# Optimization experiments

Hardware: AMD Instinct MI355X
Metric: run time of the kernel (lower is better)

Reference implementation:

```python
import jax, jax.numpy as jnp
import numpy as np

N = 50000      # nodes
E = 800000     # directed edges (avg degree 16)
IN, HID, OUT = 256, 128, 16


def setup_inputs() -> dict:
    key = jax.random.key(0)
    ks = jax.random.split(key, 8)
    x = jax.random.normal(ks[0], (N, IN), dtype=jnp.float32)
    edge_index = jax.random.randint(ks[1], (2, E), 0, N)
    W1 = jax.random.normal(ks[2], (IN, HID), dtype=jnp.float32) * (1.0 / np.sqrt(IN))
    b1 = jnp.zeros((HID,), jnp.float32)
    W2 = jax.random.normal(ks[3], (HID, HID), dtype=jnp.float32) * (1.0 / np.sqrt(HID))
    b2 = jnp.zeros((HID,), jnp.float32)
    Wc = jax.random.normal(ks[4], (HID, OUT), dtype=jnp.float32) * (1.0 / np.sqrt(HID))
    bc = jnp.zeros((OUT,), jnp.float32)
    return {"x": x, "W1": W1, "b1": b1, "W2": W2, "b2": b2,
            "Wc": Wc, "bc": bc, "edge_index": edge_index, "conv_time": 30}


def _gcn_norm(edge_index, n, dtype):
    # add self-loops, compute symmetric GCN normalization D^{-1/2}(A+I)D^{-1/2}
    loops = jnp.arange(n)
    src = jnp.concatenate([edge_index[0], loops])
    dst = jnp.concatenate([edge_index[1], loops])
    deg = jax.ops.segment_sum(jnp.ones_like(dst, dtype=dtype), dst, num_segments=n)
    dinv = jnp.where(deg > 0, jax.lax.rsqrt(deg), jnp.zeros_like(deg))
    norm = dinv[src] * dinv[dst]          # [E+N] edge weights
    return src, dst, norm


def _propagate(h, src, dst, norm, n, hops):
    # hops is a static Python int (conv_time)
    for _ in range(hops):
        h = jax.ops.segment_sum(h[src] * norm[:, None], dst, num_segments=n)
    return h


def reference(x, W1, b1, W2, b2, Wc, bc, edge_index, conv_time):
    n = x.shape[0]
    src, dst, norm = _gcn_norm(edge_index, n, x.dtype)
    # conv1: linear only (conv_time = 0)
    h = jax.nn.relu(x @ W1 + b1)
    # dropout is identity in eval mode
    # conv2: linear + conv_time hops of normalized propagation
    h = _propagate(h @ W2 + b2, src, dst, norm, n, int(conv_time))
    h = jax.nn.relu(h)
    # cls: linear + 1 hop
    h = _propagate(h @ Wc + bc, src, dst, norm, n, 1)
    return h
```

## Files before the change

kernel.cpp:

```cpp
#include <hip/hip_runtime.h>
#include <hip/hip_fp16.h>

#define NNODES 50000
#define NEDGES 800000
#define IN_F   256
#define HID_F  128
#define OUT_F  16
#define HOPS   30
#define MPAD   50048

typedef unsigned int u32;
typedef _Float16 f16;
typedef f16 f16x8 __attribute__((ext_vector_type(8)));
typedef float f32x4 __attribute__((ext_vector_type(4)));

union U32H2 { u32 u; __half2 h; };

__device__ inline float2 upk(u32 v) {
    U32H2 t; t.u = v;
    return __half22float2(t.h);
}
__device__ inline u32 pk2(float a, float b) {
    U32H2 t; t.h = __floats2half2_rn(a, b);
    return t.u;
}


__global__ void k_init_deg(int* __restrict__ deg, int n) {
    int i = blockIdx.x * blockDim.x + threadIdx.x;
    if (i < n) deg[i] = 1;
}

__global__ void k_count(const int* __restrict__ dst, int* __restrict__ deg, int e) {
    int i = blockIdx.x * blockDim.x + threadIdx.x;
    if (i < e) atomicAdd(&deg[dst[i]], 1);
}

__global__ void k_dinv(const int* __restrict__ deg, float* __restrict__ dinv, int n) {
    int i = blockIdx.x * blockDim.x + threadIdx.x;
    if (i < n) dinv[i] = rsqrtf((float)deg[i]);
}

__global__ void k_scan1(const int* __restrict__ deg, int* __restrict__ bsums, int n) {
    __shared__ int sh[256];
    int tid = threadIdx.x;
    int i = blockIdx.x * 256 + tid;
    sh[tid] = (i < n) ? deg[i] : 0;
    __syncthreads();
    for (int ofs = 128; ofs > 0; ofs >>= 1) {
        if (tid < ofs) sh[tid] += sh[tid + ofs];
        __syncthreads();
    }
    if (tid == 0) bsums[blockIdx.x] = sh[0];
}

__global__ void k_scan2(int* __restrict__ bsums, int nb, int* __restrict__ rp, int n) {
    if (threadIdx.x == 0 && blockIdx.x == 0) {
        int run = 0;
        for (int b = 0; b < nb; ++b) { int t = bsums[b]; bsums[b] = run; run += t; }
        rp[n] = run;
    }
}

__global__ void k_scan3(const int* __restrict__ deg, const int* __restrict__ bsums,
                        int* __restrict__ rp, int* __restrict__ cursor, int n) {
    __shared__ int sh[256];
    int tid = threadIdx.x;
    int i = blockIdx.x * 256 + tid;
    int v = (i < n) ? deg[i] : 0;
    sh[tid] = v;
    __syncthreads();
    for (int ofs = 1; ofs < 256; ofs <<= 1) {
        int t = 0;
        if (tid >= ofs) t = sh[tid - ofs];
        __syncthreads();
        sh[tid] += t;
        __syncthreads();
    }
    if (i < n) {
        int excl = sh[tid] - v + bsums[blockIdx.x];
        rp[i] = excl;
        cursor[i] = excl;
    }
}

__global__ void k_scatter(const int* __restrict__ src, const int* __restrict__ dst,
                          const float* __restrict__ dinv, int* __restrict__ cursor,
                          int2* __restrict__ ew, int e, int n) {
    int t = blockIdx.x * blockDim.x + threadIdx.x;
    if (t < e) {
        int s = src[t], d = dst[t];
        int pos = atomicAdd(&cursor[d], 1);
        ew[pos] = make_int2(s, __float_as_int(dinv[s] * dinv[d]));
    } else if (t < e + n) {
        int i = t - e;
        int pos = atomicAdd(&cursor[i], 1);
        float di = dinv[i];
        ew[pos] = make_int2(i, __float_as_int(di * di));
    }
}

__global__ void k_sortwave(const int* __restrict__ rp, int2* __restrict__ ew, int n) {
    int node = blockIdx.x * 4 + (threadIdx.x >> 6);
    int lane = threadIdx.x & 63;
    if (node >= n) return;
    int beg = rp[node], end = rp[node + 1];
    int deg = end - beg;
    if (deg > 64) return;
    int2 my = make_int2(0x7fffffff, 0);
    if (lane < deg) my = ew[beg + lane];
    int rank = 0;
#pragma unroll 8
    for (int k = 0; k < 64; ++k) {
        int sk = __shfl(my.x, k);
        rank += (sk < my.x) || (sk == my.x && k < lane);
    }
    if (lane < deg) ew[beg + rank] = my;
}


__global__ void k_cast_x(const float* __restrict__ in, f16* __restrict__ out, int n) {
    int i = blockIdx.x * blockDim.x + threadIdx.x;
    int stride = gridDim.x * blockDim.x;
    for (; i < n / 4; i += stride) {
        float4 v = reinterpret_cast<const float4*>(in)[i];
        f16 o[4] = {(f16)v.x, (f16)v.y, (f16)v.z, (f16)v.w};
        *reinterpret_cast<uint2*>(&reinterpret_cast<f16*>(out)[i * 4]) =
            *reinterpret_cast<uint2*>(o);
    }
}

template<int K, int NC>
__global__ void k_cast_wt(const float* __restrict__ W, f16* __restrict__ Wt) {
    int i = blockIdx.x * blockDim.x + threadIdx.x;
    if (i < K * NC) {
        int k = i / NC, c = i % NC;
        Wt[(size_t)c * K + k] = (f16)W[i];
    }
}


template<int K, bool RELU>
__global__ __launch_bounds__(256)
void k_gemm_mfma(const f16* __restrict__ A, const f16* __restrict__ Wt,
                 const float* __restrict__ b, f16* __restrict__ C, int M) {
    int wid  = threadIdx.x >> 6;
    int lane = threadIdx.x & 63;
    int rowW = blockIdx.x * 64 + wid * 16;
    int rl   = lane & 15;
    int kc   = (lane >> 4) * 8;

    f32x4 acc[8];
#pragma unroll
    for (int n = 0; n < 8; ++n) acc[n] = (f32x4)0.f;

    const f16* Arow = A + (size_t)(rowW + rl) * K;
#pragma unroll
    for (int k0 = 0; k0 < K; k0 += 32) {
        f16x8 aF = *reinterpret_cast<const f16x8*>(Arow + k0 + kc);
#pragma unroll
        for (int n = 0; n < 8; ++n) {
            f16x8 bF = *reinterpret_cast<const f16x8*>(
                Wt + (size_t)(n * 16 + rl) * K + k0 + kc);
            acc[n] = __builtin_amdgcn_mfma_f32_16x16x32_f16(aF, bF, acc[n], 0, 0, 0);
        }
    }

#pragma unroll
    for (int n = 0; n < 8; ++n) {
        int col = n * 16 + rl;
        float bias = b[col];
#pragma unroll
        for (int j = 0; j < 4; ++j) {
            int row = rowW + 4 * (lane >> 4) + j;
            if (row < M) {
                float s = acc[n][j] + bias;
                if (RELU) s = fmaxf(s, 0.f);
                C[(size_t)row * 128 + col] = (f16)s;
            }
        }
    }
}


template<bool RELU>
__global__ void k_proph(const u32* __restrict__ Hin, u32* __restrict__ Hout,
                        const int* __restrict__ rp, const int2* __restrict__ ew,
                        int n) {
    int grp  = threadIdx.x >> 4;
    int lane = threadIdx.x & 15;
    int node = blockIdx.x * 16 + grp;
    if (node >= n) return;
    int beg = rp[node], end = rp[node + 1];
    const uint4* H4 = reinterpret_cast<const uint4*>(Hin);

    float acc[8];
#pragma unroll
    for (int i = 0; i < 8; ++i) acc[i] = 0.f;

    auto body = [&](int e) {
        int2 p   = ew[e];
        float ww = __int_as_float(p.y);
        uint4 v  = H4[(size_t)p.x * 16 + lane];
        const u32* vv = reinterpret_cast<const u32*>(&v);
#pragma unroll
        for (int q = 0; q < 4; ++q) {
            float2 f = upk(vv[q]);
            acc[q * 2 + 0] += ww * f.x;
            acc[q * 2 + 1] += ww * f.y;
        }
    };

    int e = beg;
    for (; e + 1 < end; e += 2) { body(e); body(e + 1); }
    if (e < end) body(e);

    if (RELU) {
#pragma unroll
        for (int i = 0; i < 8; ++i) acc[i] = fmaxf(acc[i], 0.f);
    }
    uint4 o;
    u32* ov = reinterpret_cast<u32*>(&o);
#pragma unroll
    for (int q = 0; q < 4; ++q) ov[q] = pk2(acc[q * 2], acc[q * 2 + 1]);
    reinterpret_cast<uint4*>(Hout)[(size_t)node * 16 + lane] = o;
}


__global__ void k_cls_h(const u32* __restrict__ Ah, const float* __restrict__ Wc,
                        const float* __restrict__ bc, float* __restrict__ G, int M) {
    __shared__ float sa[64][132];
    __shared__ float4 sw4[512];
    int tid  = threadIdx.x;
    int row0 = blockIdx.x * 64;

    for (int idx = tid; idx < 512; idx += 256)
        sw4[idx] = reinterpret_cast<const float4*>(Wc)[idx];

    const uint4* A4 = reinterpret_cast<const uint4*>(Ah);
    for (int idx = tid; idx < 64 * 16; idx += 256) {
        int r = idx >> 4, c = idx & 15;
        int gr = row0 + r;
        uint4 v = (gr < M) ? A4[(size_t)gr * 16 + c]
                           : make_uint4(0u, 0u, 0u, 0u);
        float* dst = &sa[r][c * 8];
        const u32* vv = reinterpret_cast<const u32*>(&v);
#pragma unroll
        for (int q = 0; q < 4; ++q) {
            float2 f = upk(vv[q]);
            dst[q * 2 + 0] = f.x;
            dst[q * 2 + 1] = f.y;
        }
    }
    __syncthreads();

    int tc = tid & 3;
    int tr = tid >> 2;
    float4 acc = make_float4(0.f, 0.f, 0.f, 0.f);
    for (int k4 = 0; k4 < 32; ++k4) {
        float4 a = *reinterpret_cast<const float4*>(&sa[tr][k4 * 4]);
        const float* af = reinterpret_cast<const float*>(&a);
#pragma unroll
        for (int kk = 0; kk < 4; ++kk) {
            float4 wv = sw4[(k4 * 4 + kk) * 4 + tc];
            float av = af[kk];
            acc.x += av * wv.x; acc.y += av * wv.y;
            acc.z += av * wv.z; acc.w += av * wv.w;
        }
    }
    int r = row0 + tr;
    if (r < M) {
        float4 bb = reinterpret_cast<const float4*>(bc)[tc];
        acc.x += bb.x; acc.y += bb.y; acc.z += bb.z; acc.w += bb.w;
        reinterpret_cast<float4*>(G)[(size_t)r * 4 + tc] = acc;
    }
}


__global__ void k_prop16(const float* __restrict__ Gin, float* __restrict__ Out,
                         const int* __restrict__ rp, const int2* __restrict__ ew,
                         int n) {
    int g    = blockIdx.x * 64 + (threadIdx.x >> 2);
    int lane = threadIdx.x & 3;
    if (g >= n) return;
    int beg = rp[g], end = rp[g + 1];
    const float4* G4 = reinterpret_cast<const float4*>(Gin);
    float ax = 0.f, ay = 0.f, az = 0.f, aw = 0.f;
    for (int e = beg; e < end; ++e) {
        int2 p   = ew[e];
        float ww = __int_as_float(p.y);
        float4 hv = G4[(size_t)p.x * 4 + lane];
        ax += ww * hv.x; ay += ww * hv.y; az += ww * hv.z; aw += ww * hv.w;
    }
    reinterpret_cast<float4*>(Out)[(size_t)g * 4 + lane] = make_float4(ax, ay, az, aw);
}


extern "C" void kernel_launch(void* const* d_in, const int* in_sizes, int n_in,
                              void* d_out, int out_size, void* d_ws, size_t ws_size,
                              hipStream_t stream) {
    const float* x  = (const float*)d_in[0];
    const float* W1 = (const float*)d_in[1];
    const float* b1 = (const float*)d_in[2];
    const float* W2 = (const float*)d_in[3];
    const float* b2 = (const float*)d_in[4];
    const float* Wc = (const float*)d_in[5];
    const float* bc = (const float*)d_in[6];
    const int*   ei = (const int*)d_in[7];
    const int* srcp = ei;
    const int* dstp = ei + NEDGES;
    float* out = (float*)d_out;

    char* p = (char*)d_ws;
    auto alloc = [&](size_t bytes) -> char* {
        char* r = p;
        p += (bytes + 255) & ~(size_t)255;
        return r;
    };
    int*   deg    = (int*)  alloc(NNODES * 4);
    float* dinv   = (float*)alloc(NNODES * 4);
    int*   rp     = (int*)  alloc((NNODES + 1) * 4);
    int*   cursor = (int*)  alloc(NNODES * 4);
    int*   bsums  = (int*)  alloc(256 * 4);
    int2*  ew     = (int2*) alloc((size_t)(NEDGES + NNODES) * 8);
    f16*   xh     = (f16*)  alloc((size_t)MPAD * IN_F * 2);
    f16*   W1t    = (f16*)  alloc((size_t)HID_F * IN_F * 2);
    f16*   W2t    = (f16*)  alloc((size_t)HID_F * HID_F * 2);
    f16*   H0h    = (f16*)  alloc((size_t)MPAD * HID_F * 2);
    u32*   Hh0    = (u32*)  alloc((size_t)NNODES * HID_F * 2);
    u32*   Hh1    = (u32*)  alloc((size_t)NNODES * HID_F * 2);
    float* G      = (float*)alloc((size_t)NNODES * OUT_F * 4);

    const int T = 256;
    auto nb = [](int n, int t) { return (n + t - 1) / t; };

    k_init_deg<<<nb(NNODES, T), T, 0, stream>>>(deg, NNODES);
    k_count<<<nb(NEDGES, T), T, 0, stream>>>(dstp, deg, NEDGES);
    k_dinv<<<nb(NNODES, T), T, 0, stream>>>(deg, dinv, NNODES);
    int NB = nb(NNODES, 256);
    k_scan1<<<NB, 256, 0, stream>>>(deg, bsums, NNODES);
    k_scan2<<<1, 1, 0, stream>>>(bsums, NB, rp, NNODES);
    k_scan3<<<NB, 256, 0, stream>>>(deg, bsums, rp, cursor, NNODES);
    k_scatter<<<nb(NEDGES + NNODES, T), T, 0, stream>>>(srcp, dstp, dinv, cursor,
                                                        ew, NEDGES, NNODES);
    k_sortwave<<<nb(NNODES, 4), 256, 0, stream>>>(rp, ew, NNODES);

    k_cast_x<<<1024, 256, 0, stream>>>(x, xh, NNODES * IN_F);
    k_cast_wt<IN_F,  HID_F><<<nb(IN_F * HID_F, T), T, 0, stream>>>(W1, W1t);
    k_cast_wt<HID_F, HID_F><<<nb(HID_F * HID_F, T), T, 0, stream>>>(W2, W2t);

    int GB = MPAD / 64;
    k_gemm_mfma<IN_F,  true ><<<GB, 256, 0, stream>>>(xh,  W1t, b1, H0h, NNODES);
    k_gemm_mfma<HID_F, false><<<GB, 256, 0, stream>>>(H0h, W2t, b2, (f16*)Hh0, NNODES);

    u32* cur = Hh0;
    u32* nxt = Hh1;
    int PB = nb(NNODES, 16);
    for (int i = 0; i < HOPS; ++i) {
        if (i == HOPS - 1)
            k_proph<true ><<<PB, 256, 0, stream>>>(cur, nxt, rp, ew, NNODES);
        else
            k_proph<false><<<PB, 256, 0, stream>>>(cur, nxt, rp, ew, NNODES);
        u32* t = cur; cur = nxt; nxt = t;
    }

    k_cls_h<<<nb(NNODES, 64), 256, 0, stream>>>(cur, Wc, bc, G, NNODES);
    k_prop16<<<nb(NNODES, 64), 256, 0, stream>>>(G, out, rp, ew, NNODES);
}
```

Baseline: 1.122 ms.

## Fuse x cast into GEMM, defer edge weights to sort, nontemporal hop loads

```diff
diff --git a/kernel.cpp b/kernel.cpp
--- a/kernel.cpp
+++ b/kernel.cpp
@@ -10,9 +10,11 @@
 #define MPAD   50048
 
 typedef unsigned int u32;
+typedef unsigned long long u64;
 typedef _Float16 f16;
 typedef f16 f16x8 __attribute__((ext_vector_type(8)));
 typedef float f32x4 __attribute__((ext_vector_type(4)));
+typedef u32 u32x4 __attribute__((ext_vector_type(4)));
 
 union U32H2 { u32 u; __half2 h; };
 
@@ -85,48 +87,43 @@
 }
 
 __global__ void k_scatter(const int* __restrict__ src, const int* __restrict__ dst,
-                          const float* __restrict__ dinv, int* __restrict__ cursor,
-                          int2* __restrict__ ew, int e, int n) {
+                          int* __restrict__ cursor, int* __restrict__ es,
+                          int e, int n) {
     int t = blockIdx.x * blockDim.x + threadIdx.x;
     if (t < e) {
-        int s = src[t], d = dst[t];
-        int pos = atomicAdd(&cursor[d], 1);
-        ew[pos] = make_int2(s, __float_as_int(dinv[s] * dinv[d]));
+        int pos = atomicAdd(&cursor[dst[t]], 1);
+        es[pos] = src[t];
     } else if (t < e + n) {
         int i = t - e;
         int pos = atomicAdd(&cursor[i], 1);
-        float di = dinv[i];
-        ew[pos] = make_int2(i, __float_as_int(di * di));
-    }
-}
-
-__global__ void k_sortwave(const int* __restrict__ rp, int2* __restrict__ ew, int n) {
+        es[pos] = i;
+    }
+}
+
+__global__ void k_sortwave(const int* __restrict__ rp, const int* __restrict__ es,
+                           const float* __restrict__ dinv, int2* __restrict__ ew,
+                           int n) {
     int node = blockIdx.x * 4 + (threadIdx.x >> 6);
     int lane = threadIdx.x & 63;
     if (node >= n) return;
     int beg = rp[node], end = rp[node + 1];
     int deg = end - beg;
-    if (deg > 64) return;
-    int2 my = make_int2(0x7fffffff, 0);
-    if (lane < deg) my = ew[beg + lane];
-    int rank = 0;
-#pragma unroll 8
-    for (int k = 0; k < 64; ++k) {
-        int sk = __shfl(my.x, k);
-        rank += (sk < my.x) || (sk == my.x && k < lane);
-    }
-    if (lane < deg) ew[beg + rank] = my;
-}
-
-
-__global__ void k_cast_x(const float* __restrict__ in, f16* __restrict__ out, int n) {
-    int i = blockIdx.x * blockDim.x + threadIdx.x;
-    int stride = gridDim.x * blockDim.x;
-    for (; i < n / 4; i += stride) {
-        float4 v = reinterpret_cast<const float4*>(in)[i];
-        f16 o[4] = {(f16)v.x, (f16)v.y, (f16)v.z, (f16)v.w};
-        *reinterpret_cast<uint2*>(&reinterpret_cast<f16*>(out)[i * 4]) =
-            *reinterpret_cast<uint2*>(o);
+    float dd = dinv[node];
+    if (deg <= 64) {
+        int s = 0x7fffffff;
+        if (lane < deg) s = es[beg + lane];
+        int rank = 0;
+        for (int k = 0; k < deg; ++k) {
+            int sk = __shfl(s, k);
+            rank += (sk < s) || (sk == s && k < lane);
+        }
+        if (lane < deg)
+            ew[beg + rank] = make_int2(s, __float_as_int(dinv[s] * dd));
+    } else {
+        for (int t = beg + lane; t < end; t += 64) {
+            int s = es[t];
+            ew[t] = make_int2(s, __float_as_int(dinv[s] * dd));
+        }
     }
 }
 
@@ -140,9 +137,9 @@
 }
 
 
-template<int K, bool RELU>
+template<int K, bool RELU, typename TA>
 __global__ __launch_bounds__(256)
-void k_gemm_mfma(const f16* __restrict__ A, const f16* __restrict__ Wt,
+void k_gemm_mfma(const TA* __restrict__ A, const f16* __restrict__ Wt,
                  const float* __restrict__ b, f16* __restrict__ C, int M) {
     int wid  = threadIdx.x >> 6;
     int lane = threadIdx.x & 63;
@@ -154,10 +151,20 @@
 #pragma unroll
     for (int n = 0; n < 8; ++n) acc[n] = (f32x4)0.f;
 
-    const f16* Arow = A + (size_t)(rowW + rl) * K;
+    int ar = rowW + rl;
+    if (ar >= M) ar = M - 1;
+    const TA* Arow = A + (size_t)ar * K;
 #pragma unroll
     for (int k0 = 0; k0 < K; k0 += 32) {
-        f16x8 aF = *reinterpret_cast<const f16x8*>(Arow + k0 + kc);
+        f16x8 aF;
+        if constexpr (sizeof(TA) == 4) {
+            float4 v0 = *reinterpret_cast<const float4*>(Arow + k0 + kc);
+            float4 v1 = *reinterpret_cast<const float4*>(Arow + k0 + kc + 4);
+            aF[0] = (f16)v0.x; aF[1] = (f16)v0.y; aF[2] = (f16)v0.z; aF[3] = (f16)v0.w;
+            aF[4] = (f16)v1.x; aF[5] = (f16)v1.y; aF[6] = (f16)v1.z; aF[7] = (f16)v1.w;
+        } else {
+            aF = *reinterpret_cast<const f16x8*>(Arow + k0 + kc);
+        }
 #pragma unroll
         for (int n = 0; n < 8; ++n) {
             f16x8 bF = *reinterpret_cast<const f16x8*>(
@@ -192,20 +199,21 @@
     int node = blockIdx.x * 16 + grp;
     if (node >= n) return;
     int beg = rp[node], end = rp[node + 1];
-    const uint4* H4 = reinterpret_cast<const uint4*>(Hin);
+    const u32x4* H4 = reinterpret_cast<const u32x4*>(Hin);
+    const u64* ew8  = reinterpret_cast<const u64*>(ew);
 
     float acc[8];
 #pragma unroll
     for (int i = 0; i < 8; ++i) acc[i] = 0.f;
 
     auto body = [&](int e) {
-        int2 p   = ew[e];
-        float ww = __int_as_float(p.y);
-        uint4 v  = H4[(size_t)p.x * 16 + lane];
-        const u32* vv = reinterpret_cast<const u32*>(&v);
+        u64 pw   = __builtin_nontemporal_load(ew8 + e);
+        int s    = (int)(u32)pw;
+        float ww = __int_as_float((u32)(pw >> 32));
+        u32x4 v  = H4[(size_t)s * 16 + lane];
 #pragma unroll
         for (int q = 0; q < 4; ++q) {
-            float2 f = upk(vv[q]);
+            float2 f = upk(v[q]);
             acc[q * 2 + 0] += ww * f.x;
             acc[q * 2 + 1] += ww * f.y;
         }
@@ -219,11 +227,11 @@
 #pragma unroll
         for (int i = 0; i < 8; ++i) acc[i] = fmaxf(acc[i], 0.f);
     }
-    uint4 o;
-    u32* ov = reinterpret_cast<u32*>(&o);
-#pragma unroll
-    for (int q = 0; q < 4; ++q) ov[q] = pk2(acc[q * 2], acc[q * 2 + 1]);
-    reinterpret_cast<uint4*>(Hout)[(size_t)node * 16 + lane] = o;
+    u32x4 o;
+#pragma unroll
+    for (int q = 0; q < 4; ++q) o[q] = pk2(acc[q * 2], acc[q * 2 + 1]);
+    __builtin_nontemporal_store(o, reinterpret_cast<u32x4*>(Hout) +
+                                       ((size_t)node * 16 + lane));
 }
 
 
@@ -322,12 +330,12 @@
     int*   rp     = (int*)  alloc((NNODES + 1) * 4);
     int*   cursor = (int*)  alloc(NNODES * 4);
     int*   bsums  = (int*)  alloc(256 * 4);
+    int*   es     = (int*)  alloc((size_t)(NEDGES + NNODES) * 4);
     int2*  ew     = (int2*) alloc((size_t)(NEDGES + NNODES) * 8);
-    f16*   xh     = (f16*)  alloc((size_t)MPAD * IN_F * 2);
     f16*   W1t    = (f16*)  alloc((size_t)HID_F * IN_F * 2);
     f16*   W2t    = (f16*)  alloc((size_t)HID_F * HID_F * 2);
     f16*   H0h    = (f16*)  alloc((size_t)MPAD * HID_F * 2);
-    u32*   Hh0    = (u32*)  alloc((size_t)NNODES * HID_F * 2);
+    u32*   Hh0    = (u32*)  alloc((size_t)MPAD * HID_F * 2);
     u32*   Hh1    = (u32*)  alloc((size_t)NNODES * HID_F * 2);
     float* G      = (float*)alloc((size_t)NNODES * OUT_F * 4);
 
@@ -341,17 +349,16 @@
     k_scan1<<<NB, 256, 0, stream>>>(deg, bsums, NNODES);
     k_scan2<<<1, 1, 0, stream>>>(bsums, NB, rp, NNODES);
     k_scan3<<<NB, 256, 0, stream>>>(deg, bsums, rp, cursor, NNODES);
-    k_scatter<<<nb(NEDGES + NNODES, T), T, 0, stream>>>(srcp, dstp, dinv, cursor,
-                                                        ew, NEDGES, NNODES);
-    k_sortwave<<<nb(NNODES, 4), 256, 0, stream>>>(rp, ew, NNODES);
-
-    k_cast_x<<<1024, 256, 0, stream>>>(x, xh, NNODES * IN_F);
+    k_scatter<<<nb(NEDGES + NNODES, T), T, 0, stream>>>(srcp, dstp, cursor, es,
+                                                        NEDGES, NNODES);
+    k_sortwave<<<nb(NNODES, 4), 256, 0, stream>>>(rp, es, dinv, ew, NNODES);
+
     k_cast_wt<IN_F,  HID_F><<<nb(IN_F * HID_F, T), T, 0, stream>>>(W1, W1t);
     k_cast_wt<HID_F, HID_F><<<nb(HID_F * HID_F, T), T, 0, stream>>>(W2, W2t);
 
     int GB = MPAD / 64;
-    k_gemm_mfma<IN_F,  true ><<<GB, 256, 0, stream>>>(xh,  W1t, b1, H0h, NNODES);
-    k_gemm_mfma<HID_F, false><<<GB, 256, 0, stream>>>(H0h, W2t, b2, (f16*)Hh0, NNODES);
+    k_gemm_mfma<IN_F,  true,  float><<<GB, 256, 0, stream>>>(x,   W1t, b1, H0h, NNODES);
+    k_gemm_mfma<HID_F, false, f16  ><<<GB, 256, 0, stream>>>(H0h, W2t, b2, (f16*)Hh0, NNODES);
 
     u32* cur = Hh0;
     u32* nxt = Hh1;
```

Result: slower. 1.369 ms (+22.0%).
